# Kernel optimization log

Hardware: AMD Instinct MI355X
Metric: run time of the kernel (lower is better)

The kernel has to match this reference:

```python
import jax, jax.numpy as jnp
import numpy as np

D_MODEL = 1024
HEADS = 16
D_K = D_MODEL // HEADS
D_FF = 4096
EPS = 1e-5


def _layernorm(x, gamma, beta):
    mu = jnp.mean(x, axis=-1, keepdims=True)
    var = jnp.var(x, axis=-1, keepdims=True)
    return (x - mu) * jax.lax.rsqrt(var + EPS) * gamma + beta


def setup_inputs() -> dict:
    key = jax.random.key(0)
    ks = jax.random.split(key, 8)
    s = 0.02
    return {
        "x": jax.random.normal(ks[0], (4, 2048, D_MODEL), dtype=jnp.float32),
        "wq": jax.random.normal(ks[1], (D_MODEL, D_MODEL), dtype=jnp.float32) * s,
        "wk": jax.random.normal(ks[2], (D_MODEL, D_MODEL), dtype=jnp.float32) * s,
        "wv": jax.random.normal(ks[3], (D_MODEL, D_MODEL), dtype=jnp.float32) * s,
        "wo": jax.random.normal(ks[4], (D_MODEL, D_MODEL), dtype=jnp.float32) * s,
        "w1": jax.random.normal(ks[5], (D_MODEL, D_FF), dtype=jnp.float32) * s,
        "b1": jnp.zeros((D_FF,), dtype=jnp.float32),
        "w2": jax.random.normal(ks[6], (D_FF, D_MODEL), dtype=jnp.float32) * s,
        "b2": jnp.zeros((D_MODEL,), dtype=jnp.float32),
        "g1": jnp.ones((D_MODEL,), dtype=jnp.float32),
        "be1": jnp.zeros((D_MODEL,), dtype=jnp.float32),
        "g2": jnp.ones((D_MODEL,), dtype=jnp.float32),
        "be2": jnp.zeros((D_MODEL,), dtype=jnp.float32),
    }


def reference(x, wq, wk, wv, wo, w1, b1, w2, b2, g1, be1, g2, be2):
    B, S, D = x.shape
    # --- multi-head self-attention (dropout = identity at eval) ---
    q = (x @ wq).reshape(B, S, HEADS, D_K).transpose(0, 2, 1, 3)  # [B,H,S,dk]
    k = (x @ wk).reshape(B, S, HEADS, D_K).transpose(0, 2, 1, 3)
    v = (x @ wv).reshape(B, S, HEADS, D_K).transpose(0, 2, 1, 3)
    scores = jnp.einsum("bhqd,bhkd->bhqk", q, k) / jnp.sqrt(jnp.float32(D_K))
    attn = jax.nn.softmax(scores, axis=-1)
    ctx = jnp.einsum("bhqk,bhkd->bhqd", attn, v)
    ctx = ctx.transpose(0, 2, 1, 3).reshape(B, S, D)
    attn_out = ctx @ wo
    # --- add & norm 1 ---
    h = _layernorm(x + attn_out, g1, be1)
    # --- FFN ---
    ffn = jax.nn.relu(h @ w1 + b1) @ w2 + b2
    # --- add & norm 2 ---
    return _layernorm(h + ffn, g2, be2)
```

## Files before the change

### kernel.cpp

```cpp
#include <hip/hip_runtime.h>
#include <hip/hip_bf16.h>


typedef float  floatx2  __attribute__((ext_vector_type(2)));
typedef float  floatx4  __attribute__((ext_vector_type(4)));
typedef float  floatx16 __attribute__((ext_vector_type(16)));
typedef short  shortx8  __attribute__((ext_vector_type(8)));
typedef short  shortx4  __attribute__((ext_vector_type(4)));
typedef int    intx4    __attribute__((ext_vector_type(4)));
typedef unsigned uintx2 __attribute__((ext_vector_type(2)));

__device__ __forceinline__ short f2bs(float f) {
    union { float f; unsigned u; } a; a.f = f;
    unsigned r = a.u + 0x7fffu + ((a.u >> 16) & 1u);
    return (short)(r >> 16);
}

__device__ __forceinline__ float fexp2(float x) {
#if __has_builtin(__builtin_amdgcn_exp2f)
    return __builtin_amdgcn_exp2f(x);
#else
    return __expf(0.6931471805599453f * x);
#endif
}

__device__ __forceinline__ void lane32swap(unsigned& a, unsigned& b) {
#if __has_builtin(__builtin_amdgcn_permlane32_swap)
    uintx2 r = __builtin_amdgcn_permlane32_swap(a, b, false, false);
    a = r[0]; b = r[1];
#else
    int hl = (threadIdx.x & 63) >> 5;
    unsigned ta = (unsigned)__shfl_xor((int)a, 32);
    unsigned tb = (unsigned)__shfl_xor((int)b, 32);
    unsigned na = hl ? tb : a;
    unsigned nb = hl ? b : ta;
    a = na; b = nb;
#endif
}

__device__ __forceinline__ void gload16(const short* g, short* l) {
    __builtin_amdgcn_global_load_lds(
        (const __attribute__((address_space(1))) void*)g,
        (__attribute__((address_space(3))) void*)l,
        16, 0, 0);
}

#define WAITV(n) asm volatile("s_waitcnt vmcnt(" #n ")" ::: "memory")
#define FENCE    asm volatile("" ::: "memory")

__device__ __forceinline__ void trans_tile(const float* __restrict__ in,
                                           short* __restrict__ out,
                                           int N, int K, int k0, int n0,
                                           short (*t)[68]) {
    const int tid = threadIdx.x;
    const int r = tid >> 4, c4 = (tid & 15) * 4;
#pragma unroll
    for (int i = 0; i < 4; ++i) {
        int k = r + i * 16;
        floatx4 v = *(const floatx4*)(in + (size_t)(k0 + k) * N + n0 + c4);
        shortx4 s;
#pragma unroll
        for (int j = 0; j < 4; ++j) s[j] = f2bs(v[j]);
        *(shortx4*)(&t[k][c4]) = s;
    }
    __syncthreads();
#pragma unroll
    for (int i = 0; i < 4; ++i) {
        int n = r + i * 16;
        shortx4 s;
#pragma unroll
        for (int j = 0; j < 4; ++j) s[j] = t[c4 + j][n];
        *(shortx4*)(out + (size_t)(n0 + n) * K + k0 + c4) = s;
    }
}

__global__ __launch_bounds__(256) void prep_kernel(
    const float* __restrict__ wq, const float* __restrict__ wk,
    const float* __restrict__ wv, const float* __restrict__ wo,
    const float* __restrict__ w1, const float* __restrict__ w2,
    const float* __restrict__ x,
    short* wqt, short* wkt, short* wvt, short* wot,
    short* w1t, short* w2t, short* xb)
{
    __shared__ __align__(16) short t[64][68];
    const int bid = blockIdx.x;
    if (bid < 1024) {
        const int widx = bid >> 8, local = bid & 255;
        const float* in = widx == 0 ? wq : widx == 1 ? wk : widx == 2 ? wv : wo;
        short* out = widx == 0 ? wqt : widx == 1 ? wkt : widx == 2 ? wvt : wot;
        trans_tile(in, out, 1024, 1024, (local & 15) * 64, (local >> 4) * 64, t);
    } else if (bid < 2048) {
        const int local = bid - 1024;
        trans_tile(w1, w1t, 4096, 1024, (local & 15) * 64, (local >> 4) * 64, t);
    } else if (bid < 3072) {
        const int local = bid - 2048;
        trans_tile(w2, w2t, 1024, 4096, (local & 63) * 64, (local >> 6) * 64, t);
    } else {
        const int local = bid - 3072;
#pragma unroll
        for (int j = 0; j < 4; ++j) {
            int i = local * 1024 + j * 256 + threadIdx.x;
            floatx4 v = *(const floatx4*)(x + (size_t)i * 4);
            shortx4 o;
            o[0] = f2bs(v[0]); o[1] = f2bs(v[1]); o[2] = f2bs(v[2]); o[3] = f2bs(v[3]);
            *(shortx4*)(xb + (size_t)i * 4) = o;
        }
    }
}

template<int EPI, int BN>
__global__ __launch_bounds__(512, 2) void gemm256(
    const short* __restrict__ A, const short* __restrict__ Bt, const int K, const int N,
    short* __restrict__ outb, float* __restrict__ outf,
    const float* __restrict__ bias, const float* __restrict__ resf)
{
    constexpr int BUFSZ = 16384 + BN * 64;
    constexpr int NF = BN / 64;
    __shared__ __align__(16) short Ls[2 * BUFSZ];
    const int tid = threadIdx.x;
    const int w = tid >> 6, lane = tid & 63;
    const int quad = lane >> 4, l16 = lane & 15;
    const int wm = w >> 2, wn = w & 3;
    const int bx = blockIdx.x, by = blockIdx.y;

    const int srow = w * 16 + (lane >> 3);
    const int uc0 = ((lane & 7) ^ ((lane >> 4) & 7)) * 8;
    const int uc1 = ((lane & 7) ^ (((lane >> 4) + 4) & 7)) * 8;
    const short* aS0 = A  + (size_t)(by * 256 + srow) * K + uc0;
    const short* aS1 = A  + (size_t)(by * 256 + srow + 8) * K + uc1;
    const short* bS0 = Bt + (size_t)(bx * BN + srow) * K + uc0;
    const short* bS1 = Bt + (size_t)(bx * BN + srow + 8) * K + uc1;
    const size_t hK = (size_t)128 * K;
    const int wsl = w * 1024;

    const int rswz = (l16 >> 1) & 7;
    const int ru0 = (quad ^ rswz) * 8;
    const int ru1 = ((4 + quad) ^ rswz) * 8;
    const int aRd = (wm * 64 + l16) * 64;
    const int bRd = (wn * 32 + l16) * 64;

    floatx4 acc[8][NF] = {};
    shortx8 af[4][2], blo[2][2], bhi[2][2];

#define S_A0(buf, kc) { short* p = Ls + (buf) * BUFSZ + wsl;         gload16(aS0 + (kc), p);      gload16(aS1 + (kc), p + 512);      FENCE; }
#define S_A1(buf, kc) { short* p = Ls + (buf) * BUFSZ + 8192 + wsl;  gload16(aS0 + hK + (kc), p); gload16(aS1 + hK + (kc), p + 512); FENCE; }
#define S_B0(buf, kc) { short* p = Ls + (buf) * BUFSZ + 16384 + wsl; gload16(bS0 + (kc), p);      gload16(bS1 + (kc), p + 512);      FENCE; }
#define S_B1(buf, kc) { short* p = Ls + (buf) * BUFSZ + 24576 + wsl; gload16(bS0 + hK + (kc), p); gload16(bS1 + hK + (kc), p + 512); FENCE; }
#define MF(a, b, c) c = __builtin_amdgcn_mfma_f32_16x16x32_bf16(a, b, c, 0, 0, 0)

    const int NT = K >> 6;

    if constexpr (BN == 256) {
        S_A0(0, 0) S_B0(0, 0) S_B1(0, 0) S_A1(0, 0)
        for (int t = 0; t < NT - 1; ++t) {
            const int rb = t & 1, wbuf = rb ^ 1, kc = (t + 1) * 64;
            const short* Ab = Ls + rb * BUFSZ;
            const short* Bb = Ab + 16384;
            WAITV(4); __builtin_amdgcn_s_barrier(); FENCE;
#pragma unroll
            for (int mf = 0; mf < 4; ++mf) {
                af[mf][0] = *(const shortx8*)(Ab + aRd + mf * 1024 + ru0);
                af[mf][1] = *(const shortx8*)(Ab + aRd + mf * 1024 + ru1);
            }
#pragma unroll
            for (int nf = 0; nf < 2; ++nf) {
                blo[nf][0] = *(const shortx8*)(Bb + bRd + nf * 1024 + ru0);
                blo[nf][1] = *(const shortx8*)(Bb + bRd + nf * 1024 + ru1);
            }
            S_A0(wbuf, kc)
            __builtin_amdgcn_s_setprio(1);
#pragma unroll
            for (int mf = 0; mf < 4; ++mf)
#pragma unroll
                for (int nf = 0; nf < 2; ++nf) {
                    MF(af[mf][0], blo[nf][0], acc[mf][nf]);
                    MF(af[mf][1], blo[nf][1], acc[mf][nf]);
                }
            __builtin_amdgcn_s_setprio(0);
            WAITV(4); __builtin_amdgcn_s_barrier(); FENCE;
#pragma unroll
            for (int nf = 0; nf < 2; ++nf) {
                bhi[nf][0] = *(const shortx8*)(Bb + bRd + 8192 + nf * 1024 + ru0);
                bhi[nf][1] = *(const shortx8*)(Bb + bRd + 8192 + nf * 1024 + ru1);
            }
            S_B0(wbuf, kc)
            __builtin_amdgcn_s_setprio(1);
#pragma unroll
            for (int mf = 0; mf < 4; ++mf)
#pragma unroll
                for (int nf = 0; nf < 2; ++nf) {
                    MF(af[mf][0], bhi[nf][0], acc[mf][2 + nf]);
                    MF(af[mf][1], bhi[nf][1], acc[mf][2 + nf]);
                }
            __builtin_amdgcn_s_setprio(0);
            WAITV(4); __builtin_amdgcn_s_barrier(); FENCE;
#pragma unroll
            for (int mf = 0; mf < 4; ++mf) {
                af[mf][0] = *(const shortx8*)(Ab + aRd + 8192 + mf * 1024 + ru0);
                af[mf][1] = *(const shortx8*)(Ab + aRd + 8192 + mf * 1024 + ru1);
            }
            S_B1(wbuf, kc)
            __builtin_amdgcn_s_setprio(1);
#pragma unroll
            for (int mf = 0; mf < 4; ++mf)
#pragma unroll
                for (int nf = 0; nf < 2; ++nf) {
                    MF(af[mf][0], blo[nf][0], acc[4 + mf][nf]);
                    MF(af[mf][1], blo[nf][1], acc[4 + mf][nf]);
                }
            __builtin_amdgcn_s_setprio(0);
            S_A1(wbuf, kc)
            __builtin_amdgcn_s_setprio(1);
#pragma unroll
            for (int mf = 0; mf < 4; ++mf)
#pragma unroll
                for (int nf = 0; nf < 2; ++nf) {
                    MF(af[mf][0], bhi[nf][0], acc[4 + mf][2 + nf]);
                    MF(af[mf][1], bhi[nf][1], acc[4 + mf][2 + nf]);
                }
            __builtin_amdgcn_s_setprio(0);
        }
        {
            const int rb = (NT - 1) & 1;
            const short* Ab = Ls + rb * BUFSZ;
            const short* Bb = Ab + 16384;
            WAITV(4); __builtin_amdgcn_s_barrier(); FENCE;
#pragma unroll
            for (int mf = 0; mf < 4; ++mf) {
                af[mf][0] = *(const shortx8*)(Ab + aRd + mf * 1024 + ru0);
                af[mf][1] = *(const shortx8*)(Ab + aRd + mf * 1024 + ru1);
            }
#pragma unroll
            for (int nf = 0; nf < 2; ++nf) {
                blo[nf][0] = *(const shortx8*)(Bb + bRd + nf * 1024 + ru0);
                blo[nf][1] = *(const shortx8*)(Bb + bRd + nf * 1024 + ru1);
            }
            __builtin_amdgcn_s_setprio(1);
#pragma unroll
            for (int mf = 0; mf < 4; ++mf)
#pragma unroll
                for (int nf = 0; nf < 2; ++nf) {
                    MF(af[mf][0], blo[nf][0], acc[mf][nf]);
                    MF(af[mf][1], blo[nf][1], acc[mf][nf]);
                }
            __builtin_amdgcn_s_setprio(0);
            WAITV(2); __builtin_amdgcn_s_barrier(); FENCE;
#pragma unroll
            for (int nf = 0; nf < 2; ++nf) {
                bhi[nf][0] = *(const shortx8*)(Bb + bRd + 8192 + nf * 1024 + ru0);
                bhi[nf][1] = *(const shortx8*)(Bb + bRd + 8192 + nf * 1024 + ru1);
            }
            __builtin_amdgcn_s_setprio(1);
#pragma unroll
            for (int mf = 0; mf < 4; ++mf)
#pragma unroll
                for (int nf = 0; nf < 2; ++nf) {
                    MF(af[mf][0], bhi[nf][0], acc[mf][2 + nf]);
                    MF(af[mf][1], bhi[nf][1], acc[mf][2 + nf]);
                }
            __builtin_amdgcn_s_setprio(0);
            WAITV(0); __builtin_amdgcn_s_barrier(); FENCE;
#pragma unroll
            for (int mf = 0; mf < 4; ++mf) {
                af[mf][0] = *(const shortx8*)(Ab + aRd + 8192 + mf * 1024 + ru0);
                af[mf][1] = *(const shortx8*)(Ab + aRd + 8192 + mf * 1024 + ru1);
            }
            __builtin_amdgcn_s_setprio(1);
#pragma unroll
            for (int mf = 0; mf < 4; ++mf)
#pragma unroll
                for (int nf = 0; nf < 2; ++nf) {
                    MF(af[mf][0], blo[nf][0], acc[4 + mf][nf]);
                    MF(af[mf][1], blo[nf][1], acc[4 + mf][nf]);
                    MF(af[mf][0], bhi[nf][0], acc[4 + mf][2 + nf]);
                    MF(af[mf][1], bhi[nf][1], acc[4 + mf][2 + nf]);
                }
            __builtin_amdgcn_s_setprio(0);
        }
    } else {
        S_A0(0, 0) S_B0(0, 0) S_A1(0, 0)
        for (int t = 0; t < NT - 1; ++t) {
            const int rb = t & 1, wbuf = rb ^ 1, kc = (t + 1) * 64;
            const short* Ab = Ls + rb * BUFSZ;
            const short* Bb = Ab + 16384;
            WAITV(2); __builtin_amdgcn_s_barrier(); FENCE;
#pragma unroll
            for (int mf = 0; mf < 4; ++mf) {
                af[mf][0] = *(const shortx8*)(Ab + aRd + mf * 1024 + ru0);
                af[mf][1] = *(const shortx8*)(Ab + aRd + mf * 1024 + ru1);
            }
#pragma unroll
            for (int nf = 0; nf < 2; ++nf) {
                blo[nf][0] = *(const shortx8*)(Bb + bRd + nf * 1024 + ru0);
                blo[nf][1] = *(const shortx8*)(Bb + bRd + nf * 1024 + ru1);
            }
            S_A0(wbuf, kc)
            __builtin_amdgcn_s_setprio(1);
#pragma unroll
            for (int mf = 0; mf < 4; ++mf)
#pragma unroll
                for (int nf = 0; nf < 2; ++nf) {
                    MF(af[mf][0], blo[nf][0], acc[mf][nf]);
                    MF(af[mf][1], blo[nf][1], acc[mf][nf]);
                }
            __builtin_amdgcn_s_setprio(0);
            WAITV(2); __builtin_amdgcn_s_barrier(); FENCE;
#pragma unroll
            for (int mf = 0; mf < 4; ++mf) {
                af[mf][0] = *(const shortx8*)(Ab + aRd + 8192 + mf * 1024 + ru0);
                af[mf][1] = *(const shortx8*)(Ab + aRd + 8192 + mf * 1024 + ru1);
            }
            S_B0(wbuf, kc) S_A1(wbuf, kc)
            __builtin_amdgcn_s_setprio(1);
#pragma unroll
            for (int mf = 0; mf < 4; ++mf)
#pragma unroll
                for (int nf = 0; nf < 2; ++nf) {
                    MF(af[mf][0], blo[nf][0], acc[4 + mf][nf]);
                    MF(af[mf][1], blo[nf][1], acc[4 + mf][nf]);
                }
            __builtin_amdgcn_s_setprio(0);
        }
        {
            const int rb = (NT - 1) & 1;
            const short* Ab = Ls + rb * BUFSZ;
            const short* Bb = Ab + 16384;
            WAITV(2); __builtin_amdgcn_s_barrier(); FENCE;
#pragma unroll
            for (int mf = 0; mf < 4; ++mf) {
                af[mf][0] = *(const shortx8*)(Ab + aRd + mf * 1024 + ru0);
                af[mf][1] = *(const shortx8*)(Ab + aRd + mf * 1024 + ru1);
            }
#pragma unroll
            for (int nf = 0; nf < 2; ++nf) {
                blo[nf][0] = *(const shortx8*)(Bb + bRd + nf * 1024 + ru0);
                blo[nf][1] = *(const shortx8*)(Bb + bRd + nf * 1024 + ru1);
            }
            __builtin_amdgcn_s_setprio(1);
#pragma unroll
            for (int mf = 0; mf < 4; ++mf)
#pragma unroll
                for (int nf = 0; nf < 2; ++nf) {
                    MF(af[mf][0], blo[nf][0], acc[mf][nf]);
                    MF(af[mf][1], blo[nf][1], acc[mf][nf]);
                }
            __builtin_amdgcn_s_setprio(0);
            WAITV(0); __builtin_amdgcn_s_barrier(); FENCE;
#pragma unroll
            for (int mf = 0; mf < 4; ++mf) {
                af[mf][0] = *(const shortx8*)(Ab + aRd + 8192 + mf * 1024 + ru0);
                af[mf][1] = *(const shortx8*)(Ab + aRd + 8192 + mf * 1024 + ru1);
            }
            __builtin_amdgcn_s_setprio(1);
#pragma unroll
            for (int mf = 0; mf < 4; ++mf)
#pragma unroll
                for (int nf = 0; nf < 2; ++nf) {
                    MF(af[mf][0], blo[nf][0], acc[4 + mf][nf]);
                    MF(af[mf][1], blo[nf][1], acc[4 + mf][nf]);
                }
            __builtin_amdgcn_s_setprio(0);
        }
    }

#pragma unroll
    for (int mf = 0; mf < 8; ++mf) {
        const int grow0 = by * 256 + (mf >> 2) * 128 + wm * 64 + (mf & 3) * 16 + quad * 4;
#pragma unroll
        for (int nf = 0; nf < NF; ++nf) {
            int gcol;
            if constexpr (BN == 256)
                gcol = bx * 256 + (nf >> 1) * 128 + wn * 32 + (nf & 1) * 16 + l16;
            else
                gcol = bx * 128 + wn * 32 + nf * 16 + l16;
            const floatx4 a = acc[mf][nf];
            if constexpr (EPI == 5) {
                const int slice = gcol >> 10, c = gcol & 1023;
                const int hh = c >> 6, d = c & 63;
                const int b = grow0 >> 11, s0 = grow0 & 2047;
                if (slice == 2) {
                    short* vt = outb + ((size_t)16 << 20);
                    shortx4 pkv;
#pragma unroll
                    for (int r = 0; r < 4; ++r) pkv[r] = f2bs(a[r]);
                    *(shortx4*)(vt + ((size_t)((b * 16 + hh) * 64 + d)) * 2048 + s0) = pkv;
                } else {
                    short* dst = slice ? (outb + ((size_t)8 << 20)) : outb;
                    float sc = slice ? 1.f : 0.125f * 1.4426950408889634f;
#pragma unroll
                    for (int r = 0; r < 4; ++r)
                        dst[(((size_t)(b * 16 + hh)) * 2048 + (s0 + r)) * 64 + d] =
                            f2bs(a[r] * sc);
                }
            } else if constexpr (EPI == 1) {
                const float bv = bias[gcol];
#pragma unroll
                for (int r = 0; r < 4; ++r) {
                    float v = fmaxf(a[r] + bv, 0.f);
                    outb[(size_t)(grow0 + r) * N + gcol] = f2bs(v);
                }
            } else if constexpr (EPI == 2) {
#pragma unroll
                for (int r = 0; r < 4; ++r)
                    outf[(size_t)(grow0 + r) * N + gcol] =
                        a[r] + resf[(size_t)(grow0 + r) * N + gcol];
            } else if constexpr (EPI == 3) {
                const float bv = bias[gcol];
#pragma unroll
                for (int r = 0; r < 4; ++r)
                    outf[(size_t)(grow0 + r) * N + gcol] =
                        a[r] + bv + resf[(size_t)(grow0 + r) * N + gcol];
            }
        }
    }
#undef S_A0
#undef S_A1
#undef S_B0
#undef S_B1
#undef MF
}

__global__ __launch_bounds__(256) void ln_kernel(
    const float* __restrict__ in, float* __restrict__ outf, short* __restrict__ outb,
    const float* __restrict__ g, const float* __restrict__ be, int writeB)
{
    __shared__ float red[8];
    const int row = blockIdx.x, tid = threadIdx.x;
    const float* p = in + (size_t)row * 1024;
    floatx4 v = *(const floatx4*)(p + tid * 4);
    float s = v[0] + v[1] + v[2] + v[3];
    float q = v[0] * v[0] + v[1] * v[1] + v[2] * v[2] + v[3] * v[3];
#pragma unroll
    for (int off = 32; off; off >>= 1) {
        s += __shfl_xor(s, off);
        q += __shfl_xor(q, off);
    }
    int w = tid >> 6, lane = tid & 63;
    if (lane == 0) { red[w] = s; red[4 + w] = q; }
    __syncthreads();
    s = red[0] + red[1] + red[2] + red[3];
    q = red[4] + red[5] + red[6] + red[7];
    float mean = s * (1.f / 1024.f);
    float var = q * (1.f / 1024.f) - mean * mean;
    float rs = rsqrtf(var + 1e-5f);
    floatx4 gv = *(const floatx4*)(g + tid * 4);
    floatx4 bv = *(const floatx4*)(be + tid * 4);
    floatx4 o4;
#pragma unroll
    for (int i = 0; i < 4; ++i) o4[i] = (v[i] - mean) * rs * gv[i] + bv[i];
    *(floatx4*)(outf + (size_t)row * 1024 + tid * 4) = o4;
    if (writeB) {
        shortx4 ob;
#pragma unroll
        for (int i = 0; i < 4; ++i) ob[i] = f2bs(o4[i]);
        *(shortx4*)(outb + (size_t)row * 1024 + tid * 4) = ob;
    }
}

__global__ __launch_bounds__(256, 4) void attn_kernel(
    const short* __restrict__ Q, const short* __restrict__ K,
    const short* __restrict__ Vt, short* __restrict__ ctx)
{
    __shared__ __align__(16) short Ls[16384];
    short* Ks = Ls;
    short* Vs = Ls + 8192;
    const int tid = threadIdx.x;
    const int q0 = blockIdx.x * 128, bh = blockIdx.y;
    const int w = tid >> 6, lane = tid & 63, l31 = lane & 31, hl = lane >> 5;
    const size_t sb = (size_t)bh * 2048 * 64;

    shortx8 qf[4];
#pragma unroll
    for (int ks = 0; ks < 4; ++ks)
        qf[ks] = *(const shortx8*)(Q + sb + (size_t)(q0 + w * 32 + l31) * 64 + ks * 16 + hl * 8);

    const short* kSrc = K + sb + (size_t)(w * 32 + (lane >> 3)) * 64
                        + (((lane & 7) ^ ((lane >> 3) & 7)) * 8);
    int vOff[4];
#pragma unroll
    for (int j = 0; j < 4; ++j)
        vOff[j] = (w * 16 + j * 4 + (lane >> 4)) * 2048
                  + (((lane & 15) ^ (j * 4 + (lane >> 4))) * 8);
    const short* vBase = Vt + sb;

    const int kx = l31 & 7, vx = l31 & 15;

    floatx16 o[2] = {};
    floatx2 rsA = {0.f, 0.f}, rsB = {0.f, 0.f};
    const floatx16 z = {};

#define LD_AK(mt, ks) (*(const shortx8*)(Ks + ((mt) * 32 + l31) * 64 + ((((ks) * 2 + hl) ^ kx)) * 8))
#define LD_AV(mtd, mt, ksl) (*(const shortx8*)(Vs + ((mtd) * 32 + l31) * 128 + ((((mt) * 4 + (ksl) * 2 + hl) ^ vx)) * 8))

    for (int kt = 0; kt < 16; ++kt) {
        const int kv0 = kt * 128;
        __syncthreads();
#pragma unroll
        for (int j = 0; j < 4; ++j)
            gload16(kSrc + (size_t)kv0 * 64 + j * 512, Ks + (w * 4 + j) * 512);
#pragma unroll
        for (int j = 0; j < 4; ++j)
            gload16(vBase + vOff[j] + kv0, Vs + (w * 4 + j) * 512);
        WAITV(0);
        __syncthreads();

#pragma unroll
        for (int mt = 0; mt < 4; ++mt) {
            floatx16 sc;
            __builtin_amdgcn_s_setprio(1);
            sc = __builtin_amdgcn_mfma_f32_32x32x16_bf16(LD_AK(mt, 0), qf[0], z, 0, 0, 0);
            sc = __builtin_amdgcn_mfma_f32_32x32x16_bf16(LD_AK(mt, 1), qf[1], sc, 0, 0, 0);
            sc = __builtin_amdgcn_mfma_f32_32x32x16_bf16(LD_AK(mt, 2), qf[2], sc, 0, 0, 0);
            sc = __builtin_amdgcn_mfma_f32_32x32x16_bf16(LD_AK(mt, 3), qf[3], sc, 0, 0, 0);
            __builtin_amdgcn_s_setprio(0);
            floatx2 ps2[8];
#pragma unroll
            for (int i = 0; i < 8; ++i) {
                ps2[i][0] = fexp2(sc[2 * i]);
                ps2[i][1] = fexp2(sc[2 * i + 1]);
            }
#pragma unroll
            for (int i = 0; i < 8; i += 2) { rsA += ps2[i]; rsB += ps2[i + 1]; }
            unsigned pk[8];
#pragma unroll
            for (int i = 0; i < 8; ++i) {
                union { __hip_bfloat162 h; unsigned u; } cv;
                cv.h = __float22bfloat162_rn(make_float2(ps2[i][0], ps2[i][1]));
                pk[i] = cv.u;
            }
            lane32swap(pk[0], pk[2]);
            lane32swap(pk[1], pk[3]);
            lane32swap(pk[4], pk[6]);
            lane32swap(pk[5], pk[7]);
            __builtin_amdgcn_s_setprio(1);
#pragma unroll
            for (int ksl = 0; ksl < 2; ++ksl) {
                union { unsigned i[4]; shortx8 s8; } fr;
                fr.i[0] = pk[4 * ksl];     fr.i[1] = pk[4 * ksl + 1];
                fr.i[2] = pk[4 * ksl + 2]; fr.i[3] = pk[4 * ksl + 3];
#pragma unroll
                for (int mtd = 0; mtd < 2; ++mtd)
                    o[mtd] = __builtin_amdgcn_mfma_f32_32x32x16_bf16(LD_AV(mtd, mt, ksl), fr.s8, o[mtd], 0, 0, 0);
            }
            __builtin_amdgcn_s_setprio(0);
        }
    }
#undef LD_AK
#undef LD_AV

    float rsum = rsA[0] + rsA[1] + rsB[0] + rsB[1];
    float tot = rsum + __shfl_xor(rsum, 32);
    float inv = 1.f / tot;

    __syncthreads();
    short* O_lds = Ls;
#pragma unroll
    for (int mtd = 0; mtd < 2; ++mtd)
#pragma unroll
        for (int g = 0; g < 4; ++g) {
            shortx4 p4;
#pragma unroll
            for (int r = 0; r < 4; ++r) p4[r] = f2bs(o[mtd][4 * g + r] * inv);
            *(shortx4*)(O_lds + (w * 32 + l31) * 72 + mtd * 32 + g * 8 + hl * 4) = p4;
        }
    __syncthreads();
    const int b = bh >> 4, head = bh & 15;
#pragma unroll
    for (int it = 0; it < 4; ++it) {
        int idx = it * 256 + tid;
        int q = idx >> 3, ch = idx & 7;
        shortx8 v = *(const shortx8*)(O_lds + q * 72 + ch * 8);
        *(shortx8*)(ctx + ((size_t)(b * 2048 + q0 + q)) * 1024 + head * 64 + ch * 8) = v;
    }
}

extern "C" void kernel_launch(void* const* d_in, const int* in_sizes, int n_in,
                              void* d_out, int out_size, void* d_ws, size_t ws_size,
                              hipStream_t stream) {
    const float* x   = (const float*)d_in[0];
    const float* wq  = (const float*)d_in[1];
    const float* wk  = (const float*)d_in[2];
    const float* wv  = (const float*)d_in[3];
    const float* wo  = (const float*)d_in[4];
    const float* w1  = (const float*)d_in[5];
    const float* b1  = (const float*)d_in[6];
    const float* w2  = (const float*)d_in[7];
    const float* b2  = (const float*)d_in[8];
    const float* g1p = (const float*)d_in[9];
    const float* be1 = (const float*)d_in[10];
    const float* g2p = (const float*)d_in[11];
    const float* be2 = (const float*)d_in[12];
    float* out = (float*)d_out;

    char* ws = (char*)d_ws;
    const size_t MB = 1ull << 20;
    short* wqt  = (short*)(ws + 0 * MB);
    short* wkt  = (short*)(ws + 2 * MB);
    short* wvt  = (short*)(ws + 4 * MB);
    short* wot  = (short*)(ws + 6 * MB);
    short* w1t  = (short*)(ws + 8 * MB);
    short* w2t  = (short*)(ws + 16 * MB);
    short* xb   = (short*)(ws + 24 * MB);
    short* Qb   = (short*)(ws + 40 * MB);
    short* Kb   = (short*)(ws + 56 * MB);
    short* Vtg  = (short*)(ws + 72 * MB);
    short* ctxb = (short*)(ws + 88 * MB);
    float* tf   = (float*)(ws + 104 * MB);
    short* hb   = (short*)(ws + 136 * MB);
    short* f1b  = (short*)(ws + 40 * MB);

    prep_kernel<<<5120, 256, 0, stream>>>(wq, wk, wv, wo, w1, w2, x,
                                          wqt, wkt, wvt, wot, w1t, w2t, xb);

    gemm256<5, 128><<<dim3(24, 32), 512, 0, stream>>>(xb, wqt, 1024, 3072, Qb, nullptr, nullptr, nullptr);
    attn_kernel<<<dim3(16, 64), 256, 0, stream>>>(Qb, Kb, Vtg, ctxb);
    gemm256<2, 128><<<dim3(8, 32), 512, 0, stream>>>(ctxb, wot, 1024, 1024, nullptr, tf, nullptr, x);
    ln_kernel<<<8192, 256, 0, stream>>>(tf, tf, hb, g1p, be1, 1);
    gemm256<1, 256><<<dim3(16, 32), 512, 0, stream>>>(hb, w1t, 1024, 4096, f1b, nullptr, b1, nullptr);
    gemm256<3, 128><<<dim3(8, 32), 512, 0, stream>>>(f1b, w2t, 4096, 1024, nullptr, out, b2, tf);
    ln_kernel<<<8192, 256, 0, stream>>>(out, out, nullptr, g2p, be2, 0);
}
```

Baseline: 395.9 us.

## Triple-buffer LDS in BN=128 GEMM path to prefetch two K-tiles ahead

For the BN=128 GEMM variant, the shared-memory staging goes from two buffers to three, so global loads are issued two K-steps ahead. The prologue, loop bounds, wait counts and epilogue are restructured to match. Repeated read and MFMA blocks are factored into macros. The aim is to hide more global-load latency behind MFMA work, at the cost of 50% more LDS per block, which may reduce occupancy under the launch bound of 2 blocks.

```diff
diff --git a/kernel.cpp b/kernel.cpp
--- a/kernel.cpp
+++ b/kernel.cpp
@@ -116,7 +116,8 @@
 {
     constexpr int BUFSZ = 16384 + BN * 64;
     constexpr int NF = BN / 64;
-    __shared__ __align__(16) short Ls[2 * BUFSZ];
+    constexpr int NBUF = (BN == 128) ? 3 : 2;
+    __shared__ __align__(16) short Ls[NBUF * BUFSZ];
     const int tid = threadIdx.x;
     const int w = tid >> 6, lane = tid & 63;
     const int quad = lane >> 4, l16 = lane & 15;
@@ -148,6 +149,43 @@
 #define S_B1(buf, kc) { short* p = Ls + (buf) * BUFSZ + 24576 + wsl; gload16(bS0 + hK + (kc), p); gload16(bS1 + hK + (kc), p + 512); FENCE; }
 #define MF(a, b, c) c = __builtin_amdgcn_mfma_f32_16x16x32_bf16(a, b, c, 0, 0, 0)
 
+#define RD_ALO(Ab) {                                                      \
+_Pragma("unroll")                                                         \
+        for (int mf = 0; mf < 4; ++mf) {                                  \
+            af[mf][0] = *(const shortx8*)((Ab) + aRd + mf * 1024 + ru0);  \
+            af[mf][1] = *(const shortx8*)((Ab) + aRd + mf * 1024 + ru1);  \
+        } }
+#define RD_AHI(Ab) {                                                      \
+_Pragma("unroll")                                                         \
+        for (int mf = 0; mf < 4; ++mf) {                                  \
+            af[mf][0] = *(const shortx8*)((Ab) + aRd + 8192 + mf * 1024 + ru0); \
+            af[mf][1] = *(const shortx8*)((Ab) + aRd + 8192 + mf * 1024 + ru1); \
+        } }
+#define RD_BLO(Bb) {                                                      \
+_Pragma("unroll")                                                         \
+        for (int nf = 0; nf < 2; ++nf) {                                  \
+            blo[nf][0] = *(const shortx8*)((Bb) + bRd + nf * 1024 + ru0); \
+            blo[nf][1] = *(const shortx8*)((Bb) + bRd + nf * 1024 + ru1); \
+        } }
+#define MFMA_LO { __builtin_amdgcn_s_setprio(1);                          \
+_Pragma("unroll")                                                         \
+        for (int mf = 0; mf < 4; ++mf)                                    \
+_Pragma("unroll")                                                         \
+            for (int nf = 0; nf < 2; ++nf) {                              \
+                MF(af[mf][0], blo[nf][0], acc[mf][nf]);                   \
+                MF(af[mf][1], blo[nf][1], acc[mf][nf]);                   \
+            }                                                             \
+        __builtin_amdgcn_s_setprio(0); }
+#define MFMA_HI { __builtin_amdgcn_s_setprio(1);                          \
+_Pragma("unroll")                                                         \
+        for (int mf = 0; mf < 4; ++mf)                                    \
+_Pragma("unroll")                                                         \
+            for (int nf = 0; nf < 2; ++nf) {                              \
+                MF(af[mf][0], blo[nf][0], acc[4 + mf][nf]);               \
+                MF(af[mf][1], blo[nf][1], acc[4 + mf][nf]);               \
+            }                                                             \
+        __builtin_amdgcn_s_setprio(0); }
+
     const int NT = K >> 6;
 
     if constexpr (BN == 256) {
@@ -157,26 +195,9 @@
             const short* Ab = Ls + rb * BUFSZ;
             const short* Bb = Ab + 16384;
             WAITV(4); __builtin_amdgcn_s_barrier(); FENCE;
-#pragma unroll
-            for (int mf = 0; mf < 4; ++mf) {
-                af[mf][0] = *(const shortx8*)(Ab + aRd + mf * 1024 + ru0);
-                af[mf][1] = *(const shortx8*)(Ab + aRd + mf * 1024 + ru1);
-            }
-#pragma unroll
-            for (int nf = 0; nf < 2; ++nf) {
-                blo[nf][0] = *(const shortx8*)(Bb + bRd + nf * 1024 + ru0);
-                blo[nf][1] = *(const shortx8*)(Bb + bRd + nf * 1024 + ru1);
-            }
+            RD_ALO(Ab) RD_BLO(Bb)
             S_A0(wbuf, kc)
-            __builtin_amdgcn_s_setprio(1);
-#pragma unroll
-            for (int mf = 0; mf < 4; ++mf)
-#pragma unroll
-                for (int nf = 0; nf < 2; ++nf) {
-                    MF(af[mf][0], blo[nf][0], acc[mf][nf]);
-                    MF(af[mf][1], blo[nf][1], acc[mf][nf]);
-                }
-            __builtin_amdgcn_s_setprio(0);
+            MFMA_LO
             WAITV(4); __builtin_amdgcn_s_barrier(); FENCE;
 #pragma unroll
             for (int nf = 0; nf < 2; ++nf) {
@@ -194,21 +215,9 @@
                 }
             __builtin_amdgcn_s_setprio(0);
             WAITV(4); __builtin_amdgcn_s_barrier(); FENCE;
-#pragma unroll
-            for (int mf = 0; mf < 4; ++mf) {
-                af[mf][0] = *(const shortx8*)(Ab + aRd + 8192 + mf * 1024 + ru0);
-                af[mf][1] = *(const shortx8*)(Ab + aRd + 8192 + mf * 1024 + ru1);
-            }
+            RD_AHI(Ab)
             S_B1(wbuf, kc)
-            __builtin_amdgcn_s_setprio(1);
-#pragma unroll
-            for (int mf = 0; mf < 4; ++mf)
-#pragma unroll
-                for (int nf = 0; nf < 2; ++nf) {
-                    MF(af[mf][0], blo[nf][0], acc[4 + mf][nf]);
-                    MF(af[mf][1], blo[nf][1], acc[4 + mf][nf]);
-                }
-            __builtin_amdgcn_s_setprio(0);
+            MFMA_HI
             S_A1(wbuf, kc)
             __builtin_amdgcn_s_setprio(1);
 #pragma unroll
@@ -225,25 +234,8 @@
             const short* Ab = Ls + rb * BUFSZ;
             const short* Bb = Ab + 16384;
             WAITV(4); __builtin_amdgcn_s_barrier(); FENCE;
-#pragma unroll
-            for (int mf = 0; mf < 4; ++mf) {
-                af[mf][0] = *(const shortx8*)(Ab + aRd + mf * 1024 + ru0);
-                af[mf][1] = *(const shortx8*)(Ab + aRd + mf * 1024 + ru1);
-            }
-#pragma unroll
-            for (int nf = 0; nf < 2; ++nf) {
-                blo[nf][0] = *(const shortx8*)(Bb + bRd + nf * 1024 + ru0);
-                blo[nf][1] = *(const shortx8*)(Bb + bRd + nf * 1024 + ru1);
-            }
-            __builtin_amdgcn_s_setprio(1);
-#pragma unroll
-            for (int mf = 0; mf < 4; ++mf)
-#pragma unroll
-                for (int nf = 0; nf < 2; ++nf) {
-                    MF(af[mf][0], blo[nf][0], acc[mf][nf]);
-                    MF(af[mf][1], blo[nf][1], acc[mf][nf]);
-                }
-            __builtin_amdgcn_s_setprio(0);
+            RD_ALO(Ab) RD_BLO(Bb)
+            MFMA_LO
             WAITV(2); __builtin_amdgcn_s_barrier(); FENCE;
 #pragma unroll
             for (int nf = 0; nf < 2; ++nf) {
@@ -260,11 +252,7 @@
                 }
             __builtin_amdgcn_s_setprio(0);
             WAITV(0); __builtin_amdgcn_s_barrier(); FENCE;
-#pragma unroll
-            for (int mf = 0; mf < 4; ++mf) {
-                af[mf][0] = *(const shortx8*)(Ab + aRd + 8192 + mf * 1024 + ru0);
-                af[mf][1] = *(const shortx8*)(Ab + aRd + 8192 + mf * 1024 + ru1);
-            }
+            RD_AHI(Ab)
             __builtin_amdgcn_s_setprio(1);
 #pragma unroll
             for (int mf = 0; mf < 4; ++mf)
@@ -279,87 +267,41 @@
         }
     } else {
         S_A0(0, 0) S_B0(0, 0) S_A1(0, 0)
-        for (int t = 0; t < NT - 1; ++t) {
-            const int rb = t & 1, wbuf = rb ^ 1, kc = (t + 1) * 64;
+        S_A0(1, 64) S_B0(1, 64) S_A1(1, 64)
+        for (int t = 0; t < NT - 2; ++t) {
+            const int rb = t % 3, pb = (t + 2) % 3, kc = (t + 2) * 64;
+            const short* Ab = Ls + rb * BUFSZ;
+            const short* Bb = Ab + 16384;
+            WAITV(8); __builtin_amdgcn_s_barrier(); FENCE;
+            RD_ALO(Ab) RD_BLO(Bb)
+            S_A0(pb, kc)
+            MFMA_LO
+            WAITV(8); __builtin_amdgcn_s_barrier(); FENCE;
+            RD_AHI(Ab)
+            S_B0(pb, kc) S_A1(pb, kc)
+            MFMA_HI
+        }
+        {
+            const int rb = (NT - 2) % 3;
+            const short* Ab = Ls + rb * BUFSZ;
+            const short* Bb = Ab + 16384;
+            WAITV(8); __builtin_amdgcn_s_barrier(); FENCE;
+            RD_ALO(Ab) RD_BLO(Bb)
+            MFMA_LO
+            WAITV(6); __builtin_amdgcn_s_barrier(); FENCE;
+            RD_AHI(Ab)
+            MFMA_HI
+        }
+        {
+            const int rb = (NT - 1) % 3;
             const short* Ab = Ls + rb * BUFSZ;
             const short* Bb = Ab + 16384;
             WAITV(2); __builtin_amdgcn_s_barrier(); FENCE;
-#pragma unroll
-            for (int mf = 0; mf < 4; ++mf) {
-                af[mf][0] = *(const shortx8*)(Ab + aRd + mf * 1024 + ru0);
-                af[mf][1] = *(const shortx8*)(Ab + aRd + mf * 1024 + ru1);
-            }
-#pragma unroll
-            for (int nf = 0; nf < 2; ++nf) {
-                blo[nf][0] = *(const shortx8*)(Bb + bRd + nf * 1024 + ru0);
-                blo[nf][1] = *(const shortx8*)(Bb + bRd + nf * 1024 + ru1);
-            }
-            S_A0(wbuf, kc)
-            __builtin_amdgcn_s_setprio(1);
-#pragma unroll
-            for (int mf = 0; mf < 4; ++mf)
-#pragma unroll
-                for (int nf = 0; nf < 2; ++nf) {
-                    MF(af[mf][0], blo[nf][0], acc[mf][nf]);
-                    MF(af[mf][1], blo[nf][1], acc[mf][nf]);
-                }
-            __builtin_amdgcn_s_setprio(0);
-            WAITV(2); __builtin_amdgcn_s_barrier(); FENCE;
-#pragma unroll
-            for (int mf = 0; mf < 4; ++mf) {
-                af[mf][0] = *(const shortx8*)(Ab + aRd + 8192 + mf * 1024 + ru0);
-                af[mf][1] = *(const shortx8*)(Ab + aRd + 8192 + mf * 1024 + ru1);
-            }
-            S_B0(wbuf, kc) S_A1(wbuf, kc)
-            __builtin_amdgcn_s_setprio(1);
-#pragma unroll
-            for (int mf = 0; mf < 4; ++mf)
-#pragma unroll
-                for (int nf = 0; nf < 2; ++nf) {
-                    MF(af[mf][0], blo[nf][0], acc[4 + mf][nf]);
-                    MF(af[mf][1], blo[nf][1], acc[4 + mf][nf]);
-                }
-            __builtin_amdgcn_s_setprio(0);
-        }
-        {
-            const int rb = (NT - 1) & 1;
-            const short* Ab = Ls + rb * BUFSZ;
-            const short* Bb = Ab + 16384;
-            WAITV(2); __builtin_amdgcn_s_barrier(); FENCE;
-#pragma unroll
-            for (int mf = 0; mf < 4; ++mf) {
-                af[mf][0] = *(const shortx8*)(Ab + aRd + mf * 1024 + ru0);
-                af[mf][1] = *(const shortx8*)(Ab + aRd + mf * 1024 + ru1);
-            }
-#pragma unroll
-            for (int nf = 0; nf < 2; ++nf) {
-                blo[nf][0] = *(const shortx8*)(Bb + bRd + nf * 1024 + ru0);
-                blo[nf][1] = *(const shortx8*)(Bb + bRd + nf * 1024 + ru1);
-            }
-            __builtin_amdgcn_s_setprio(1);
-#pragma unroll
-            for (int mf = 0; mf < 4; ++mf)
-#pragma unroll
-                for (int nf = 0; nf < 2; ++nf) {
-                    MF(af[mf][0], blo[nf][0], acc[mf][nf]);
-                    MF(af[mf][1], blo[nf][1], acc[mf][nf]);
-                }
-            __builtin_amdgcn_s_setprio(0);
+            RD_ALO(Ab) RD_BLO(Bb)
+            MFMA_LO
             WAITV(0); __builtin_amdgcn_s_barrier(); FENCE;
-#pragma unroll
-            for (int mf = 0; mf < 4; ++mf) {
-                af[mf][0] = *(const shortx8*)(Ab + aRd + 8192 + mf * 1024 + ru0);
-                af[mf][1] = *(const shortx8*)(Ab + aRd + 8192 + mf * 1024 + ru1);
-            }
-            __builtin_amdgcn_s_setprio(1);
-#pragma unroll
-            for (int mf = 0; mf < 4; ++mf)
-#pragma unroll
-                for (int nf = 0; nf < 2; ++nf) {
-                    MF(af[mf][0], blo[nf][0], acc[4 + mf][nf]);
-                    MF(af[mf][1], blo[nf][1], acc[4 + mf][nf]);
-                }
-            __builtin_amdgcn_s_setprio(0);
+            RD_AHI(Ab)
+            MFMA_HI
         }
     }
 
@@ -418,6 +360,11 @@
 #undef S_B0
 #undef S_B1
 #undef MF
+#undef RD_ALO
+#undef RD_AHI
+#undef RD_BLO
+#undef MFMA_LO
+#undef MFMA_HI
 }
 
 __global__ __launch_bounds__(256) void ln_kernel(
```

Measured after the change: 382.9 us. -3.3%, faster.
